# Performance work log

Hardware: AMD Instinct MI355X
Metric: run time of the kernel (lower is better)

The kernel has to match this reference:

```python
import jax, jax.numpy as jnp
import numpy as np

B = 8192   # batch
S = 115    # state dim (fixed by slice layout)
E = 3072   # retrieval embed dim
C = 128    # compressed context dim
A = 23     # action dim
NE = 4096  # number of hyperedge keys
K = 10     # top-k retrieval
TAU = 1.0  # gumbel temperature
EPS = 1e-5 # layernorm eps


def _ln(x, g, b):
    m = x.mean(-1, keepdims=True)
    v = x.var(-1, keepdims=True)
    return (x - m) * jax.lax.rsqrt(v + EPS) * g + b


def _actor(ctx, extra, w1, b1, g1, be1, w2, b2, g2, be2, w3, b3):
    x = jnp.concatenate([ctx, extra], -1)
    x = jax.nn.relu(_ln(x @ w1 + b1, g1, be1))
    x = jax.nn.relu(_ln(x @ w2 + b2, g2, be2))
    return x @ w3 + b3


def setup_inputs() -> dict:
    key = jax.random.key(0)
    ks = iter(jax.random.split(key, 80))

    def W(shape):
        return jax.random.normal(next(ks), shape, jnp.float32) * (1.0 / float(np.sqrt(shape[0])))

    inp = {}
    inp["state"] = jax.random.normal(next(ks), (B, S), jnp.float32)
    u = jax.random.uniform(next(ks), (B, 4), jnp.float32, 1e-6, 1.0 - 1e-6)
    inp["gumbel_noise"] = -jnp.log(-jnp.log(u))  # standard Gumbel samples
    inp["keys"] = jax.random.normal(next(ks), (NE, E), jnp.float32)
    # state encoder 115 -> 512 -> 512 -> 3072 + LN
    inp["se_w1"] = W((S, 512)); inp["se_b1"] = jnp.zeros(512)
    inp["se_w2"] = W((512, 512)); inp["se_b2"] = jnp.zeros(512)
    inp["se_w3"] = W((512, E)); inp["se_b3"] = jnp.zeros(E)
    inp["se_g"] = jnp.ones(E); inp["se_beta"] = jnp.zeros(E)
    # context compressor 3072 -> 512 -> 128 + LN
    inp["cc_w1"] = W((E, 512)); inp["cc_b1"] = jnp.zeros(512)
    inp["cc_w2"] = W((512, C)); inp["cc_b2"] = jnp.zeros(C)
    inp["cc_g"] = jnp.ones(C); inp["cc_beta"] = jnp.zeros(C)
    # 4 actor experts, differing only in extra-slice width
    for p, e in [("a_pre", 50), ("a_scene", 20), ("a_effect", 10), ("a_rule", 15)]:
        inp[p + "_w1"] = W((C + e, C)); inp[p + "_b1"] = jnp.zeros(C)
        inp[p + "_g1"] = jnp.ones(C); inp[p + "_be1"] = jnp.zeros(C)
        inp[p + "_w2"] = W((C, C)); inp[p + "_b2"] = jnp.zeros(C)
        inp[p + "_g2"] = jnp.ones(C); inp[p + "_be2"] = jnp.zeros(C)
        inp[p + "_w3"] = W((C, A)) * 0.01; inp[p + "_b3"] = jnp.zeros(A)  # orthogonal gain=0.01 approx
    # gumbel router 115 -> 64 -> 64 -> 4
    inp["r_w1"] = W((S, 64)); inp["r_b1"] = jnp.zeros(64)
    inp["r_w2"] = W((64, 64)); inp["r_b2"] = jnp.zeros(64)
    inp["r_w3"] = W((64, 4)); inp["r_b3"] = jnp.zeros(4)
    # critic 115 -> 256 -> 256 -> 1
    inp["c_w1"] = W((S, 256)); inp["c_b1"] = jnp.zeros(256)
    inp["c_w2"] = W((256, 256)); inp["c_b2"] = jnp.zeros(256)
    inp["c_w3"] = W((256, 1)); inp["c_b3"] = jnp.zeros(1)
    return inp


def reference(state, gumbel_noise, keys, se_w1, se_b1, se_w2, se_b2, se_w3, se_b3, se_g, se_beta, cc_w1, cc_b1, cc_w2, cc_b2, cc_g, cc_beta, a_pre_w1, a_pre_b1, a_pre_g1, a_pre_be1, a_pre_w2, a_pre_b2, a_pre_g2, a_pre_be2, a_pre_w3, a_pre_b3, a_scene_w1, a_scene_b1, a_scene_g1, a_scene_be1, a_scene_w2, a_scene_b2, a_scene_g2, a_scene_be2, a_scene_w3, a_scene_b3, a_effect_w1, a_effect_b1, a_effect_g1, a_effect_be1, a_effect_w2, a_effect_b2, a_effect_g2, a_effect_be2, a_effect_w3, a_effect_b3, a_rule_w1, a_rule_b1, a_rule_g1, a_rule_be1, a_rule_w2, a_rule_b2, a_rule_g2, a_rule_be2, a_rule_w3, a_rule_b3, r_w1, r_b1, r_w2, r_b2, r_w3, r_b3, c_w1, c_b1, c_w2, c_b2, c_w3, c_b3):
    # 1) state -> query (StateEncoder)
    q = jax.nn.relu(state @ se_w1 + se_b1)
    q = jax.nn.relu(q @ se_w2 + se_b2)
    q = _ln(q @ se_w3 + se_b3, se_g, se_beta)  # (B, E)
    # 2) top-k hard retrieval from hypergraph memory (cosine sim)
    qn = q * jax.lax.rsqrt(jnp.sum(q * q, -1, keepdims=True) + 1e-12)
    kn = keys * jax.lax.rsqrt(jnp.sum(keys * keys, -1, keepdims=True) + 1e-12)
    scores = qn @ kn.T                          # (B, NE)
    _, idx = jax.lax.top_k(scores, K)           # (B, K)
    context = jnp.take(keys, idx, axis=0).mean(1)  # (B, E) mean-pool top-k raw embeddings
    # 3) compress to shared knowledge
    h = jax.nn.relu(context @ cc_w1 + cc_b1)
    shared = _ln(h @ cc_w2 + cc_b2, cc_g, cc_beta)  # (B, C)
    # 4) state slices + 4 actor experts
    belief = state[:, :50]
    location = state[:, 20:40]
    hp = state[:, 40:50]
    inv = state[:, 45:60]
    lp = _actor(shared, belief, a_pre_w1, a_pre_b1, a_pre_g1, a_pre_be1, a_pre_w2, a_pre_b2, a_pre_g2, a_pre_be2, a_pre_w3, a_pre_b3)
    ls = _actor(shared, location, a_scene_w1, a_scene_b1, a_scene_g1, a_scene_be1, a_scene_w2, a_scene_b2, a_scene_g2, a_scene_be2, a_scene_w3, a_scene_b3)
    le = _actor(shared, hp, a_effect_w1, a_effect_b1, a_effect_g1, a_effect_be1, a_effect_w2, a_effect_b2, a_effect_g2, a_effect_be2, a_effect_w3, a_effect_b3)
    lr = _actor(shared, inv, a_rule_w1, a_rule_b1, a_rule_g1, a_rule_be1, a_rule_w2, a_rule_b2, a_rule_g2, a_rule_be2, a_rule_w3, a_rule_b3)
    # 5) gumbel-softmax hard router (straight-through)
    rh = jax.nn.relu(state @ r_w1 + r_b1)
    rh = jax.nn.relu(rh @ r_w2 + r_b2)
    rl = jnp.clip(rh @ r_w3 + r_b3, -20.0, 20.0)
    y_soft = jax.nn.softmax((rl + gumbel_noise) / TAU, -1)
    y_hard = jax.nn.one_hot(jnp.argmax(y_soft, -1), 4, dtype=y_soft.dtype)
    alpha = y_soft + jax.lax.stop_gradient(y_hard - y_soft)  # (B, 4)
    # 6) combine expert logits
    all_l = jnp.stack([lp, ls, le, lr], 1)      # (B, 4, A)
    logits = jnp.einsum('bk,bka->ba', alpha, all_l)
    # critic value
    v = jax.nn.relu(state @ c_w1 + c_b1)
    v = jax.nn.relu(v @ c_w2 + c_b2)
    value = v @ c_w3 + c_b3                      # (B, 1)
    return (logits, alpha, value)
```

## Files before the change

kernel.cpp:

```cpp
#include <hip/hip_runtime.h>

constexpr int Bz = 8192;
constexpr int Sz = 115;
constexpr int Ez = 3072;
constexpr int NEz = 4096;

typedef __attribute__((ext_vector_type(8))) short short8;
typedef __attribute__((ext_vector_type(4))) float floatx4;
typedef unsigned short ushort_t;
typedef unsigned int uint_t;

__device__ __forceinline__ ushort_t f2bf(float f) {
  uint_t u = __float_as_uint(f);
  uint_t r = (u + 0x7FFFu + ((u >> 16) & 1u)) >> 16;
  return (ushort_t)r;
}
__device__ __forceinline__ float bf2f(ushort_t b) {
  uint_t u = ((uint_t)b) << 16;
  return __uint_as_float(u);
}
__device__ __forceinline__ ushort_t f2key(float v) {
  _Float16 h = (_Float16)v;
  ushort_t b = __builtin_bit_cast(ushort_t, h);
  return b ^ ((b & 0x8000u) ? 0xFFFFu : 0x8000u);
}
__device__ __forceinline__ uint_t umax_(uint_t a, uint_t b) { return a > b ? a : b; }

__device__ __forceinline__ void gload16(const ushort_t* g, ushort_t* l) {
  __builtin_amdgcn_global_load_lds(
      (__attribute__((address_space(1))) const void*)g,
      (__attribute__((address_space(3))) void*)l, 16, 0, 0);
}

template<bool RELU, bool BIAS>
__global__ __launch_bounds__(256)
void gemm128(const float* __restrict__ A, const float* __restrict__ Bm,
             const float* __restrict__ bias, float* __restrict__ C,
             int N, int Kd)
{
  __shared__ float As[16][132];
  __shared__ float Bs[16][132];
  const int t  = threadIdx.x;
  const int tx = t & 15, ty = t >> 4;
  const int row0 = blockIdx.y * 128;
  const int col0 = blockIdx.x * 128;
  const int ar = t >> 2, ac = (t & 3) * 4;
  const int bk = t >> 5, bc = (t & 31) * 4;
  const bool a4 = (Kd & 3) == 0;

  float acc[8][8];
#pragma unroll
  for (int i = 0; i < 8; ++i)
#pragma unroll
    for (int j = 0; j < 8; ++j) acc[i][j] = 0.f;

  for (int k0 = 0; k0 < Kd; k0 += 16) {
    const bool fullA = (k0 + 16 <= Kd) && a4;
    {
      const float* ap = A + (size_t)(row0 + ar) * Kd + k0 + ac;
      if (fullA) {
        float4 v0 = *(const float4*)ap;
        float4 v1 = *(const float4*)(ap + (size_t)64 * Kd);
        As[ac + 0][ar] = v0.x; As[ac + 1][ar] = v0.y;
        As[ac + 2][ar] = v0.z; As[ac + 3][ar] = v0.w;
        As[ac + 0][ar + 64] = v1.x; As[ac + 1][ar + 64] = v1.y;
        As[ac + 2][ar + 64] = v1.z; As[ac + 3][ar + 64] = v1.w;
      } else {
#pragma unroll
        for (int e = 0; e < 4; ++e) {
          const int k = k0 + ac + e;
          float v0 = 0.f, v1 = 0.f;
          if (k < Kd) { v0 = ap[e]; v1 = ap[e + (size_t)64 * Kd]; }
          As[ac + e][ar] = v0; As[ac + e][ar + 64] = v1;
        }
      }
    }
    {
      const float* bp = Bm + (size_t)(k0 + bk) * N + col0 + bc;
      if (k0 + 16 <= Kd) {
        *(float4*)&Bs[bk][bc]     = *(const float4*)bp;
        *(float4*)&Bs[bk + 8][bc] = *(const float4*)(bp + (size_t)8 * N);
      } else {
        float4 z; z.x = z.y = z.z = z.w = 0.f;
        *(float4*)&Bs[bk][bc]     = (k0 + bk     < Kd) ? *(const float4*)bp : z;
        *(float4*)&Bs[bk + 8][bc] = (k0 + bk + 8 < Kd) ? *(const float4*)(bp + (size_t)8 * N) : z;
      }
    }
    __syncthreads();
#pragma unroll
    for (int kk = 0; kk < 16; ++kk) {
      float a[8], b[8];
      *(float4*)&a[0] = *(const float4*)&As[kk][ty * 4];
      *(float4*)&a[4] = *(const float4*)&As[kk][64 + ty * 4];
      *(float4*)&b[0] = *(const float4*)&Bs[kk][tx * 4];
      *(float4*)&b[4] = *(const float4*)&Bs[kk][64 + tx * 4];
#pragma unroll
      for (int i = 0; i < 8; ++i)
#pragma unroll
        for (int j = 0; j < 8; ++j)
          acc[i][j] = fmaf(a[i], b[j], acc[i][j]);
    }
    __syncthreads();
  }

  float bv[8];
#pragma unroll
  for (int j = 0; j < 8; ++j) bv[j] = 0.f;
  if (BIAS) {
    *(float4*)&bv[0] = *(const float4*)&bias[col0 + tx * 4];
    *(float4*)&bv[4] = *(const float4*)&bias[col0 + 64 + tx * 4];
  }
#pragma unroll
  for (int i = 0; i < 8; ++i) {
    const int r = row0 + ((i < 4) ? (ty * 4 + i) : (64 + ty * 4 + i - 4));
    float o[8];
#pragma unroll
    for (int j = 0; j < 8; ++j) {
      o[j] = acc[i][j] + bv[j];
      if (RELU) o[j] = fmaxf(o[j], 0.f);
    }
    *(float4*)&C[(size_t)r * N + col0 + tx * 4]      = *(float4*)&o[0];
    *(float4*)&C[(size_t)r * N + col0 + 64 + tx * 4] = *(float4*)&o[4];
  }
}

struct GPart {
  const float* A; const float* Bm; const float* bias;
  float* C; ushort_t* Ch; ushort_t* Cl;
  int N; int Kd; int nbx;
};

__global__ __launch_bounds__(256)
void gemm128_dual(GPart g0, GPart g1)
{
  __shared__ float As[16][132];
  __shared__ float Bs[16][132];
  const int t  = threadIdx.x;
  const int tx = t & 15, ty = t >> 4;
  const bool p0 = (int)blockIdx.x < g0.nbx;
  GPart g = p0 ? g0 : g1;
  const int bx = p0 ? blockIdx.x : (blockIdx.x - g0.nbx);
  const int row0 = blockIdx.y * 128;
  const int col0 = bx * 128;
  const int Kd = g.Kd, N = g.N;
  const int ar = t >> 2, ac = (t & 3) * 4;
  const int bk = t >> 5, bc = (t & 31) * 4;
  const bool a4 = (Kd & 3) == 0;

  float acc[8][8];
#pragma unroll
  for (int i = 0; i < 8; ++i)
#pragma unroll
    for (int j = 0; j < 8; ++j) acc[i][j] = 0.f;

  for (int k0 = 0; k0 < Kd; k0 += 16) {
    const bool fullA = (k0 + 16 <= Kd) && a4;
    {
      const float* ap = g.A + (size_t)(row0 + ar) * Kd + k0 + ac;
      if (fullA) {
        float4 v0 = *(const float4*)ap;
        float4 v1 = *(const float4*)(ap + (size_t)64 * Kd);
        As[ac + 0][ar] = v0.x; As[ac + 1][ar] = v0.y;
        As[ac + 2][ar] = v0.z; As[ac + 3][ar] = v0.w;
        As[ac + 0][ar + 64] = v1.x; As[ac + 1][ar + 64] = v1.y;
        As[ac + 2][ar + 64] = v1.z; As[ac + 3][ar + 64] = v1.w;
      } else {
#pragma unroll
        for (int e = 0; e < 4; ++e) {
          const int k = k0 + ac + e;
          float v0 = 0.f, v1 = 0.f;
          if (k < Kd) { v0 = ap[e]; v1 = ap[e + (size_t)64 * Kd]; }
          As[ac + e][ar] = v0; As[ac + e][ar + 64] = v1;
        }
      }
    }
    {
      const float* bp = g.Bm + (size_t)(k0 + bk) * N + col0 + bc;
      if (k0 + 16 <= Kd) {
        *(float4*)&Bs[bk][bc]     = *(const float4*)bp;
        *(float4*)&Bs[bk + 8][bc] = *(const float4*)(bp + (size_t)8 * N);
      } else {
        float4 z; z.x = z.y = z.z = z.w = 0.f;
        *(float4*)&Bs[bk][bc]     = (k0 + bk     < Kd) ? *(const float4*)bp : z;
        *(float4*)&Bs[bk + 8][bc] = (k0 + bk + 8 < Kd) ? *(const float4*)(bp + (size_t)8 * N) : z;
      }
    }
    __syncthreads();
#pragma unroll
    for (int kk = 0; kk < 16; ++kk) {
      float a[8], b[8];
      *(float4*)&a[0] = *(const float4*)&As[kk][ty * 4];
      *(float4*)&a[4] = *(const float4*)&As[kk][64 + ty * 4];
      *(float4*)&b[0] = *(const float4*)&Bs[kk][tx * 4];
      *(float4*)&b[4] = *(const float4*)&Bs[kk][64 + tx * 4];
#pragma unroll
      for (int i = 0; i < 8; ++i)
#pragma unroll
        for (int j = 0; j < 8; ++j)
          acc[i][j] = fmaf(a[i], b[j], acc[i][j]);
    }
    __syncthreads();
  }

  float bv[8];
  *(float4*)&bv[0] = *(const float4*)&g.bias[col0 + tx * 4];
  *(float4*)&bv[4] = *(const float4*)&g.bias[col0 + 64 + tx * 4];
#pragma unroll
  for (int i = 0; i < 8; ++i) {
    const int r = row0 + ((i < 4) ? (ty * 4 + i) : (64 + ty * 4 + i - 4));
    float o[8];
#pragma unroll
    for (int j = 0; j < 8; ++j) o[j] = fmaxf(acc[i][j] + bv[j], 0.f);
    const size_t i0 = (size_t)r * N + col0 + tx * 4;
    const size_t i1 = i0 + 64;
    if (g.C) {
      *(float4*)&g.C[i0] = *(float4*)&o[0];
      *(float4*)&g.C[i1] = *(float4*)&o[4];
    }
    if (g.Ch) {
      ushort4 h0, l0, h1, l1;
      h0.x = f2bf(o[0]); l0.x = f2bf(o[0] - bf2f(h0.x));
      h0.y = f2bf(o[1]); l0.y = f2bf(o[1] - bf2f(h0.y));
      h0.z = f2bf(o[2]); l0.z = f2bf(o[2] - bf2f(h0.z));
      h0.w = f2bf(o[3]); l0.w = f2bf(o[3] - bf2f(h0.w));
      h1.x = f2bf(o[4]); l1.x = f2bf(o[4] - bf2f(h1.x));
      h1.y = f2bf(o[5]); l1.y = f2bf(o[5] - bf2f(h1.y));
      h1.z = f2bf(o[6]); l1.z = f2bf(o[6] - bf2f(h1.z));
      h1.w = f2bf(o[7]); l1.w = f2bf(o[7] - bf2f(h1.w));
      *(ushort4*)&g.Ch[i0] = h0; *(ushort4*)&g.Cl[i0] = l0;
      *(ushort4*)&g.Ch[i1] = h1; *(ushort4*)&g.Cl[i1] = l1;
    }
  }
}

template<int NSUB>
__global__ __launch_bounds__(256)
void mfma_bt(const ushort_t* __restrict__ A, const ushort_t* __restrict__ B,
             ushort_t* __restrict__ Cout, int N, int Kd)
{
  __shared__ ushort_t Al[NSUB * 4096];
  __shared__ ushort_t Bl[NSUB * 4096];
  const int t = threadIdx.x;
  const int wid = t >> 6, lane = t & 63;
  const int wr = wid >> 1, wc = wid & 1;
  const int row0 = blockIdx.y << 7;
  const int col0 = blockIdx.x << 7;
  const int srow = lane >> 2;
  const int scol = (lane & 3) * 8;

  const ushort_t* ga0 = A + (size_t)(row0 + wid * 16 + srow) * Kd + scol;
  const ushort_t* ga1 = A + (size_t)(row0 + (wid + 4) * 16 + srow) * Kd + scol;
  const ushort_t* gb0 = B + (size_t)(col0 + wid * 16 + srow) * Kd + scol;
  const ushort_t* gb1 = B + (size_t)(col0 + (wid + 4) * 16 + srow) * Kd + scol;
  ushort_t* la0 = &Al[wid * 512];
  ushort_t* la1 = &Al[(wid + 4) * 512];
  ushort_t* lb0 = &Bl[wid * 512];
  ushort_t* lb1 = &Bl[(wid + 4) * 512];

  const int mr = lane & 15, qd = lane >> 4;

  floatx4 acc[4][4];
#pragma unroll
  for (int i = 0; i < 4; ++i)
#pragma unroll
    for (int j = 0; j < 4; ++j) acc[i][j] = (floatx4){0.f, 0.f, 0.f, 0.f};

  for (int kb = 0; kb < Kd; kb += 32 * NSUB) {
#pragma unroll
    for (int tt = 0; tt < NSUB; ++tt) {
      const int ko = kb + 32 * tt;
      const int lo = tt * 4096;
      gload16(ga0 + ko, la0 + lo);
      gload16(ga1 + ko, la1 + lo);
      gload16(gb0 + ko, lb0 + lo);
      gload16(gb1 + ko, lb1 + lo);
    }
    __syncthreads();
#pragma unroll
    for (int tt = 0; tt < NSUB; ++tt) {
      const int lo = tt * 4096;
      short8 aF[4], bF[4];
#pragma unroll
      for (int i = 0; i < 4; ++i)
        aF[i] = *(const short8*)&Al[lo + (wr * 64 + i * 16 + mr) * 32 + qd * 8];
#pragma unroll
      for (int j = 0; j < 4; ++j)
        bF[j] = *(const short8*)&Bl[lo + (wc * 64 + j * 16 + mr) * 32 + qd * 8];
#pragma unroll
      for (int i = 0; i < 4; ++i)
#pragma unroll
        for (int j = 0; j < 4; ++j)
          acc[i][j] = __builtin_amdgcn_mfma_f32_16x16x32_bf16(aF[i], bF[j], acc[i][j], 0, 0, 0);
    }
    __syncthreads();
  }

#pragma unroll
  for (int i = 0; i < 4; ++i) {
#pragma unroll
    for (int j = 0; j < 4; ++j) {
      const int col = col0 + wc * 64 + j * 16 + mr;
#pragma unroll
      for (int r = 0; r < 4; ++r) {
        const int row = row0 + wr * 64 + i * 16 + qd * 4 + r;
        Cout[(size_t)row * N + col] = f2key(acc[i][j][r]);
      }
    }
  }
}

template<int EPI>
__global__ __launch_bounds__(256)
void mfma3_bt(const ushort_t* __restrict__ Ah, const ushort_t* __restrict__ Alo,
              const ushort_t* __restrict__ Bh, const ushort_t* __restrict__ Blo,
              const float* __restrict__ bias, float* __restrict__ Cout,
              ushort_t* __restrict__ Ch, ushort_t* __restrict__ Cl,
              int N, int Kd)
{
  __shared__ ushort_t AhL[128 * 32];
  __shared__ ushort_t AlL[128 * 32];
  __shared__ ushort_t BhL[128 * 32];
  __shared__ ushort_t BlL[128 * 32];
  const int t = threadIdx.x;
  const int wid = t >> 6, lane = t & 63;
  const int wr = wid >> 1, wc = wid & 1;
  const int row0 = blockIdx.y * 128;
  const int col0 = blockIdx.x * 128;
  const int srow = lane >> 2;
  const int scol = (lane & 3) * 8;

  const size_t aoff0 = (size_t)(row0 + wid * 16 + srow) * Kd + scol;
  const size_t aoff1 = (size_t)(row0 + (wid + 4) * 16 + srow) * Kd + scol;
  const size_t boff0 = (size_t)(col0 + wid * 16 + srow) * Kd + scol;
  const size_t boff1 = (size_t)(col0 + (wid + 4) * 16 + srow) * Kd + scol;
  const int l0 = (wid * 16) * 32;
  const int l1 = ((wid + 4) * 16) * 32;

  const int mr = lane & 15, qd = lane >> 4;

  floatx4 acc[4][4];
#pragma unroll
  for (int i = 0; i < 4; ++i)
#pragma unroll
    for (int j = 0; j < 4; ++j) acc[i][j] = (floatx4){0.f, 0.f, 0.f, 0.f};

  for (int kb = 0; kb < Kd; kb += 32) {
    gload16(Ah + aoff0 + kb, &AhL[l0]);
    gload16(Ah + aoff1 + kb, &AhL[l1]);
    gload16(Alo + aoff0 + kb, &AlL[l0]);
    gload16(Alo + aoff1 + kb, &AlL[l1]);
    gload16(Bh + boff0 + kb, &BhL[l0]);
    gload16(Bh + boff1 + kb, &BhL[l1]);
    gload16(Blo + boff0 + kb, &BlL[l0]);
    gload16(Blo + boff1 + kb, &BlL[l1]);
    __syncthreads();
    short8 ahF[4], alF[4], bhF[4], blF[4];
#pragma unroll
    for (int i = 0; i < 4; ++i) {
      const int o = (wr * 64 + i * 16 + mr) * 32 + qd * 8;
      ahF[i] = *(const short8*)&AhL[o];
      alF[i] = *(const short8*)&AlL[o];
    }
#pragma unroll
    for (int j = 0; j < 4; ++j) {
      const int o = (wc * 64 + j * 16 + mr) * 32 + qd * 8;
      bhF[j] = *(const short8*)&BhL[o];
      blF[j] = *(const short8*)&BlL[o];
    }
#pragma unroll
    for (int i = 0; i < 4; ++i)
#pragma unroll
      for (int j = 0; j < 4; ++j) {
        acc[i][j] = __builtin_amdgcn_mfma_f32_16x16x32_bf16(alF[i], bhF[j], acc[i][j], 0, 0, 0);
        acc[i][j] = __builtin_amdgcn_mfma_f32_16x16x32_bf16(ahF[i], blF[j], acc[i][j], 0, 0, 0);
        acc[i][j] = __builtin_amdgcn_mfma_f32_16x16x32_bf16(ahF[i], bhF[j], acc[i][j], 0, 0, 0);
      }
    __syncthreads();
  }

#pragma unroll
  for (int i = 0; i < 4; ++i) {
#pragma unroll
    for (int j = 0; j < 4; ++j) {
      const int col = col0 + wc * 64 + j * 16 + mr;
#pragma unroll
      for (int r = 0; r < 4; ++r) {
        const int row = row0 + wr * 64 + i * 16 + qd * 4 + r;
        const float v = acc[i][j][r] + bias[col];
        if (EPI == 0) {
          Cout[(size_t)row * N + col] = v;
        } else {
          const float y = fmaxf(v, 0.f);
          const ushort_t h = f2bf(y);
          Ch[(size_t)row * N + col] = h;
          Cl[(size_t)row * N + col] = f2bf(y - bf2f(h));
        }
      }
    }
  }
}

__global__ __launch_bounds__(256)
void mfma_bt64(const ushort_t* __restrict__ A, const ushort_t* __restrict__ B,
               const float* __restrict__ bias, float* __restrict__ Cout,
               int N, int Kd)
{
  __shared__ ushort_t Al[2 * 64 * 32];
  __shared__ ushort_t Bl[2 * 128 * 32];
  const int t = threadIdx.x;
  const int wid = t >> 6, lane = t & 63;
  const int row0 = blockIdx.y << 6;
  const int col0 = blockIdx.x << 7;
  const int srow = lane >> 2;
  const int scol = (lane & 3) * 8;
  const int mr = lane & 15, qd = lane >> 4;

  const ushort_t* gsrc[6];
  ushort_t* ldst[6];
#pragma unroll
  for (int m = 0; m < 6; ++m) {
    const int c = wid * 6 + m;
    if (c < 8) {
      const int sub = c >> 2, grp = c & 3;
      gsrc[m] = A + (size_t)(row0 + grp * 16 + srow) * Kd + sub * 32 + scol;
      ldst[m] = &Al[sub * 2048 + (grp * 16 + srow) * 32];
    } else {
      const int b = c - 8, sub = b >> 3, grp = b & 7;
      gsrc[m] = B + (size_t)(col0 + grp * 16 + srow) * Kd + sub * 32 + scol;
      ldst[m] = &Bl[sub * 4096 + (grp * 16 + srow) * 32];
    }
  }

  floatx4 acc[4][2];
#pragma unroll
  for (int i = 0; i < 4; ++i)
#pragma unroll
    for (int j = 0; j < 2; ++j) acc[i][j] = (floatx4){0.f, 0.f, 0.f, 0.f};

  for (int kb = 0; kb < Kd; kb += 64) {
#pragma unroll
    for (int m = 0; m < 6; ++m) gload16(gsrc[m] + kb, ldst[m]);
    __syncthreads();
#pragma unroll
    for (int sub = 0; sub < 2; ++sub) {
      short8 aF[4], bF[2];
#pragma unroll
      for (int i = 0; i < 4; ++i)
        aF[i] = *(const short8*)&Al[sub * 2048 + (i * 16 + mr) * 32 + qd * 8];
#pragma unroll
      for (int j = 0; j < 2; ++j)
        bF[j] = *(const short8*)&Bl[sub * 4096 + (wid * 32 + j * 16 + mr) * 32 + qd * 8];
#pragma unroll
      for (int i = 0; i < 4; ++i)
#pragma unroll
        for (int j = 0; j < 2; ++j)
          acc[i][j] = __builtin_amdgcn_mfma_f32_16x16x32_bf16(aF[i], bF[j], acc[i][j], 0, 0, 0);
    }
    __syncthreads();
  }

#pragma unroll
  for (int i = 0; i < 4; ++i) {
#pragma unroll
    for (int j = 0; j < 2; ++j) {
      const int col = col0 + wid * 32 + j * 16 + mr;
#pragma unroll
      for (int r = 0; r < 4; ++r) {
        const int row = row0 + i * 16 + qd * 4 + r;
        Cout[(size_t)row * N + col] = fmaxf(acc[i][j][r] + bias[col], 0.f);
      }
    }
  }
}

__global__ __launch_bounds__(256)
void gemm_scores(const float* __restrict__ A, const float* __restrict__ Bm,
                 const float* __restrict__ rk, ushort_t* __restrict__ S)
{
  __shared__ float As[16][132];
  __shared__ float Bs[16][132];
  const int t  = threadIdx.x;
  const int tx = t & 15, ty = t >> 4;
  const int row0 = blockIdx.y * 128;
  const int col0 = blockIdx.x * 128;
  const int ar = t >> 2, ac = (t & 3) * 4;
  const int Kd = Ez;

  float acc[8][8];
#pragma unroll
  for (int i = 0; i < 8; ++i)
#pragma unroll
    for (int j = 0; j < 8; ++j) acc[i][j] = 0.f;

  for (int k0 = 0; k0 < Kd; k0 += 16) {
    {
      const float* ap = A + (size_t)(row0 + ar) * Kd + k0 + ac;
      float4 v0 = *(const float4*)ap;
      float4 v1 = *(const float4*)(ap + (size_t)64 * Kd);
      As[ac + 0][ar] = v0.x; As[ac + 1][ar] = v0.y;
      As[ac + 2][ar] = v0.z; As[ac + 3][ar] = v0.w;
      As[ac + 0][ar + 64] = v1.x; As[ac + 1][ar + 64] = v1.y;
      As[ac + 2][ar + 64] = v1.z; As[ac + 3][ar + 64] = v1.w;
    }
    {
      const float* bp = Bm + (size_t)(col0 + ar) * Kd + k0 + ac;
      float4 v0 = *(const float4*)bp;
      float4 v1 = *(const float4*)(bp + (size_t)64 * Kd);
      Bs[ac + 0][ar] = v0.x; Bs[ac + 1][ar] = v0.y;
      Bs[ac + 2][ar] = v0.z; Bs[ac + 3][ar] = v0.w;
      Bs[ac + 0][ar + 64] = v1.x; Bs[ac + 1][ar + 64] = v1.y;
      Bs[ac + 2][ar + 64] = v1.z; Bs[ac + 3][ar + 64] = v1.w;
    }
    __syncthreads();
#pragma unroll
    for (int kk = 0; kk < 16; ++kk) {
      float a[8], b[8];
      *(float4*)&a[0] = *(const float4*)&As[kk][ty * 4];
      *(float4*)&a[4] = *(const float4*)&As[kk][64 + ty * 4];
      *(float4*)&b[0] = *(const float4*)&Bs[kk][tx * 4];
      *(float4*)&b[4] = *(const float4*)&Bs[kk][64 + tx * 4];
#pragma unroll
      for (int i = 0; i < 8; ++i)
#pragma unroll
        for (int j = 0; j < 8; ++j)
          acc[i][j] = fmaf(a[i], b[j], acc[i][j]);
    }
    __syncthreads();
  }

  float rk0[8];
  *(float4*)&rk0[0] = *(const float4*)&rk[col0 + tx * 4];
  *(float4*)&rk0[4] = *(const float4*)&rk[col0 + 64 + tx * 4];
#pragma unroll
  for (int i = 0; i < 8; ++i) {
    const int r = row0 + ((i < 4) ? (ty * 4 + i) : (64 + ty * 4 + i - 4));
    ushort4 h0, h1;
    h0.x = f2key(acc[i][0] * rk0[0]); h0.y = f2key(acc[i][1] * rk0[1]);
    h0.z = f2key(acc[i][2] * rk0[2]); h0.w = f2key(acc[i][3] * rk0[3]);
    h1.x = f2key(acc[i][4] * rk0[4]); h1.y = f2key(acc[i][5] * rk0[5]);
    h1.z = f2key(acc[i][6] * rk0[6]); h1.w = f2key(acc[i][7] * rk0[7]);
    *(ushort4*)&S[(size_t)r * NEz + col0 + tx * 4]      = h0;
    *(ushort4*)&S[(size_t)r * NEz + col0 + 64 + tx * 4] = h1;
  }
}

struct LN4 {
  const float* W[4]; const float* b[4]; const float* g[4]; const float* be[4];
  int eoff[4]; int elen[4];
};

template<bool RELU, bool HASEXT>
__global__ __launch_bounds__(256)
void gemm_ln4(const float* __restrict__ A1base, size_t a1stride, int K1,
              const float* __restrict__ A2, LN4 p,
              float* __restrict__ outbase, size_t ostride)
{
  __shared__ float As[32][68];
  __shared__ float Bs[32][132];
  __shared__ float rsum[64][17];
  __shared__ float rsq[64][17];
  __shared__ float stm[64], str[64];
  const int a = blockIdx.y;
  const float* A1 = A1base + (size_t)a * a1stride;
  float* out = outbase + (size_t)a * ostride;
  const float* W = p.W[a];
  const float* bias = p.b[a];
  const float* g = p.g[a];
  const float* be = p.be[a];
  const int eoff = HASEXT ? p.eoff[a] : 0;
  const int K2 = HASEXT ? p.elen[a] : 0;

  const int t = threadIdx.x;
  const int tx = t & 15, ty = t >> 4;
  const int row0 = blockIdx.x * 64;
  const int Kt = K1 + K2;
  const int ar = t >> 2, ac = (t & 3) * 8;
  const int bk = t >> 3, bc = (t & 7) * 16;

  float acc[4][8];
#pragma unroll
  for (int i = 0; i < 4; ++i)
#pragma unroll
    for (int j = 0; j < 8; ++j) acc[i][j] = 0.f;

  for (int k0 = 0; k0 < Kt; k0 += 32) {
    const int grow = row0 + ar;
#pragma unroll
    for (int e = 0; e < 8; ++e) {
      const int k = k0 + ac + e;
      float v = 0.f;
      if (k < K1)      v = A1[(size_t)grow * K1 + k];
      else if (k < Kt) v = A2[(size_t)grow * 115 + eoff + (k - K1)];
      As[ac + e][ar] = v;
    }
    {
      const int k = k0 + bk;
#pragma unroll
      for (int qd = 0; qd < 4; ++qd) {
        float4 z; z.x = z.y = z.z = z.w = 0.f;
        *(float4*)&Bs[bk][bc + 4 * qd] =
            (k < Kt) ? *(const float4*)&W[(size_t)k * 128 + bc + 4 * qd] : z;
      }
    }
    __syncthreads();
#pragma unroll
    for (int kk = 0; kk < 32; ++kk) {
      float av[4], bv2[8];
// ... 275 lines not shown
  __shared__ double sv[16];
  __shared__ int si[16];
  __shared__ int sel10[10];
  const int row = blockIdx.x, t = threadIdx.x;
  const int w = t >> 6, lane = t & 63;

  {
    const float* qr = qn + (size_t)row * Ez;
#pragma unroll
    for (int i = 0; i < 3; ++i) {
      const int c = (t << 2) + (i << 10);
      *(float4*)&qs[c] = *(const float4*)&qr[c];
    }
  }
  __syncthreads();

#pragma unroll
  for (int cc = 0; cc < 4; ++cc) {
    const int slot = w * 4 + cc;
    const int id = cand[(size_t)row * 16 + slot];
    const float* kr = keys + (size_t)id * Ez;
    double s = 0.0;
#pragma unroll
    for (int it = 0; it < 12; ++it) {
      const int c = (lane << 2) + (it << 8);
      float4 k4 = *(const float4*)&kr[c];
      float4 q4 = *(const float4*)&qs[c];
      s += (double)q4.x * (double)k4.x;
      s += (double)q4.y * (double)k4.y;
      s += (double)q4.z * (double)k4.z;
      s += (double)q4.w * (double)k4.w;
    }
#pragma unroll
    for (int d = 32; d; d >>= 1) s += __shfl_down(s, d, 64);
    if (lane == 0) { sv[slot] = s * (double)rk[id]; si[slot] = id; }
  }
  __syncthreads();

  if (t == 0) {
    for (int it = 0; it < 10; ++it) {
      int bj = 0; double bvv = sv[0]; int bi = si[0];
      for (int j = 1; j < 16; ++j) {
        const double v = sv[j]; const int i2 = si[j];
        if (v > bvv || (v == bvv && i2 < bi)) { bj = j; bvv = v; bi = i2; }
      }
      sel10[it] = bi;
      sv[bj] = -1e300;
    }
  }
  __syncthreads();

  int id[10];
#pragma unroll
  for (int j = 0; j < 10; ++j) id[j] = sel10[j];

#pragma unroll
  for (int i = 0; i < 3; ++i) {
    const int c = (t << 2) + (i << 10);
    float4 a = {0.f, 0.f, 0.f, 0.f};
#pragma unroll
    for (int j = 0; j < 10; ++j) {
      float4 v = *(const float4*)&keys[(size_t)id[j] * Ez + c];
      a.x += v.x; a.y += v.y; a.z += v.z; a.w += v.w;
    }
    if (BFOUT) {
      ushort4 o;
      o.x = f2bf(a.x * 0.1f); o.y = f2bf(a.y * 0.1f);
      o.z = f2bf(a.z * 0.1f); o.w = f2bf(a.w * 0.1f);
      *(ushort4*)&((ushort_t*)ctxOut)[(size_t)row * Ez + c] = o;
    } else {
      float4 o;
      o.x = a.x * 0.1f; o.y = a.y * 0.1f; o.z = a.z * 0.1f; o.w = a.w * 0.1f;
      *(float4*)&((float*)ctxOut)[(size_t)row * Ez + c] = o;
    }
  }
}

__global__ __launch_bounds__(256)
void router_kernel(const float* __restrict__ state, const float* __restrict__ gn,
                   const float* __restrict__ w1, const float* __restrict__ b1,
                   const float* __restrict__ w2, const float* __restrict__ b2,
                   const float* __restrict__ w3, const float* __restrict__ b3,
                   float* __restrict__ outAlpha)
{
  const int row = blockIdx.x * 256 + threadIdx.x;
  const float* sr = state + (size_t)row * Sz;
  float h1[64];
#pragma unroll
  for (int j = 0; j < 64; ++j) h1[j] = b1[j];
  for (int k = 0; k < Sz; ++k) {
    const float a = sr[k];
    const float* wr = w1 + (size_t)k * 64;
#pragma unroll
    for (int j = 0; j < 64; ++j) h1[j] = fmaf(a, wr[j], h1[j]);
  }
#pragma unroll
  for (int j = 0; j < 64; ++j) h1[j] = fmaxf(h1[j], 0.f);
  float h2[64];
#pragma unroll
  for (int j = 0; j < 64; ++j) h2[j] = b2[j];
#pragma unroll
  for (int k = 0; k < 64; ++k) {
    const float a = h1[k];
    const float* wr = w2 + (size_t)k * 64;
#pragma unroll
    for (int j = 0; j < 64; ++j) h2[j] = fmaf(a, wr[j], h2[j]);
  }
#pragma unroll
  for (int j = 0; j < 64; ++j) h2[j] = fmaxf(h2[j], 0.f);
  float z[4];
#pragma unroll
  for (int a = 0; a < 4; ++a) {
    float s = b3[a];
#pragma unroll
    for (int k = 0; k < 64; ++k) s = fmaf(h2[k], w3[k * 4 + a], s);
    s = fminf(fmaxf(s, -20.f), 20.f);
    z[a] = s + gn[(size_t)row * 4 + a];
  }
  float mz = z[0];
#pragma unroll
  for (int a = 1; a < 4; ++a) mz = fmaxf(mz, z[a]);
  float e[4]; float se = 0.f;
#pragma unroll
  for (int a = 0; a < 4; ++a) { e[a] = expf(z[a] - mz); se += e[a]; }
  const float inv = 1.f / se;
  float y[4];
#pragma unroll
  for (int a = 0; a < 4; ++a) y[a] = e[a] * inv;
  int am = 0;
#pragma unroll
  for (int a = 1; a < 4; ++a) if (y[a] > y[am]) am = a;
#pragma unroll
  for (int a = 0; a < 4; ++a) {
    const float hard = (a == am) ? 1.f : 0.f;
    outAlpha[(size_t)row * 4 + a] = y[a] + (hard - y[a]);
  }
}

__global__ __launch_bounds__(256)
void critic_head(const float* __restrict__ c2, const float* __restrict__ w3,
                 const float* __restrict__ b3, float* __restrict__ outv)
{
  const int t = threadIdx.x;
  const int w = t >> 6, lane = t & 63;
  const int row0 = blockIdx.x * 64 + w * 16;
  float wv[4];
  *(float4*)&wv[0] = *(const float4*)&w3[lane * 4];
  const float b0 = b3[0];
#pragma unroll
  for (int rr = 0; rr < 16; ++rr) {
    const int row = row0 + rr;
    float4 x = *(const float4*)&c2[(size_t)row * 256 + lane * 4];
    float s = x.x * wv[0] + x.y * wv[1] + x.z * wv[2] + x.w * wv[3];
#pragma unroll
    for (int d = 32; d; d >>= 1) s += __shfl_down(s, d, 64);
    if (lane == 0) outv[row] = s + b0;
  }
}

struct HeadP { const float* w3[4]; const float* b3[4]; };

__global__ __launch_bounds__(256)
void actor_head4(const float* __restrict__ x2g, HeadP p,
                 const float* __restrict__ alpha, float* __restrict__ outL)
{
  __shared__ float wsm[4][128 * 23];
  __shared__ float bs[4][23];
  const int t = threadIdx.x;
#pragma unroll
  for (int a = 0; a < 4; ++a) {
    for (int i = t; i < 128 * 23; i += 256) wsm[a][i] = p.w3[a][i];
    if (t < 23) bs[a][t] = p.b3[a][t];
  }
  __syncthreads();
  const int row = blockIdx.x * 32 + (t >> 3);
  const int cg = t & 7;
  float sum[3] = {0.f, 0.f, 0.f};
#pragma unroll
  for (int a = 0; a < 4; ++a) {
    const float al = alpha[(size_t)row * 4 + a];
    const float* xr = x2g + (size_t)a * Bz * 128 + (size_t)row * 128;
    float acc[3] = {0.f, 0.f, 0.f};
    for (int kk = 0; kk < 128; ++kk) {
      const float xa = xr[kk];
#pragma unroll
      for (int j = 0; j < 3; ++j) {
        const int col = cg + 8 * j;
        if (col < 23) acc[j] = fmaf(xa, wsm[a][kk * 23 + col], acc[j]);
      }
    }
#pragma unroll
    for (int j = 0; j < 3; ++j) {
      const int col = cg + 8 * j;
      if (col < 23) sum[j] += al * (acc[j] + bs[a][col]);
    }
  }
#pragma unroll
  for (int j = 0; j < 3; ++j) {
    const int col = cg + 8 * j;
    if (col < 23) outL[(size_t)row * 23 + col] = sum[j];
  }
}

extern "C" void kernel_launch(void* const* d_in, const int* in_sizes, int n_in,
                              void* d_out, int out_size, void* d_ws, size_t ws_size,
                              hipStream_t stream)
{
  const float* state  = (const float*)d_in[0];
  const float* gumbel = (const float*)d_in[1];
  const float* keys   = (const float*)d_in[2];
  const float* se_w1 = (const float*)d_in[3];
  const float* se_b1 = (const float*)d_in[4];
  const float* se_w2 = (const float*)d_in[5];
  const float* se_b2 = (const float*)d_in[6];
  const float* se_w3 = (const float*)d_in[7];
  const float* se_b3 = (const float*)d_in[8];
  const float* se_g  = (const float*)d_in[9];
  const float* se_be = (const float*)d_in[10];
  const float* cc_w1 = (const float*)d_in[11];
  const float* cc_b1 = (const float*)d_in[12];
  const float* cc_w2 = (const float*)d_in[13];
  const float* cc_b2 = (const float*)d_in[14];
  const float* cc_g  = (const float*)d_in[15];
  const float* cc_be = (const float*)d_in[16];
  const float* r_w1 = (const float*)d_in[57];
  const float* r_b1 = (const float*)d_in[58];
  const float* r_w2 = (const float*)d_in[59];
  const float* r_b2 = (const float*)d_in[60];
  const float* r_w3 = (const float*)d_in[61];
  const float* r_b3 = (const float*)d_in[62];
  const float* c_w1 = (const float*)d_in[63];
  const float* c_b1 = (const float*)d_in[64];
  const float* c_w2 = (const float*)d_in[65];
  const float* c_b2 = (const float*)d_in[66];
  const float* c_w3 = (const float*)d_in[67];
  const float* c_b3 = (const float*)d_in[68];

  float* wsf = (float*)d_ws;
  const size_t qF = (size_t)Bz * Ez;
  const size_t uF = (size_t)16777216;
  float* q = wsf;
  float* U = wsf + qF;
  ushort_t* sAh  = (ushort_t*)(U + 0);
  ushort_t* sAl  = (ushort_t*)(U + 2097152);
  ushort_t* sBh  = (ushort_t*)(U + 4194304);
  ushort_t* sBl  = (ushort_t*)(U + 6291456);
  ushort_t* w3hT = (ushort_t*)(U + 8388608);
  ushort_t* w3lT = (ushort_t*)(U + 9175040);
  ushort_t* w2hT = (ushort_t*)(U + 9961472);
  ushort_t* w2lT = (ushort_t*)(U + 10092544);
  float* sA = U;
  float* sB = U + 4194304;
  ushort_t* scoresU = (ushort_t*)U;
  ushort_t* ctxb = (ushort_t*)U;
  float* cch = U + 12582912;
  float* shr = U;
  float* x1g = U + 1 * 1048576;
  float* x2g = U + 5 * 1048576;
  float* cr1 = q;
  float* cr2 = q + 2097152;
  ushort_t* qbf  = (ushort_t*)(wsf + qF + uF);
  ushort_t* knbf = qbf + qF;
  ushort_t* w1T  = knbf + (size_t)NEz * Ez;
  const size_t bfHalves = qF + (size_t)NEz * Ez + (size_t)512 * Ez;
  const size_t baseBytes = (qF + uF) * sizeof(float);
  const size_t tailBytes = 4096 * 4 + (size_t)Bz * 16 * 4;
  const bool fast = ws_size >= baseBytes + bfHalves * 2 + tailBytes;
  float* tailF = (float*)((char*)d_ws + (fast ? baseBytes + bfHalves * 2 : baseBytes));
  float* rk  = tailF;
  int* cand  = (int*)(tailF + 4096);

  float* outL = (float*)d_out;
  float* outA = outL + (size_t)Bz * 23;
  float* outV = outA + (size_t)Bz * 4;

  const dim3 blk(256);

  {
    GPart e0 = {state, se_w1, se_b1, fast ? nullptr : sA,
                fast ? sAh : nullptr, fast ? sAl : nullptr, 512, 115, 4};
    GPart e1 = {state, c_w1, c_b1, cr1, nullptr, nullptr, 256, 115, 2};
    gemm128_dual<<<dim3(6, 64), blk, 0, stream>>>(e0, e1);
  }
  gemm128<true, true><<<dim3(2, 64), blk, 0, stream>>>(cr1, c_w2, c_b2, cr2, 256, 256);

  if (fast) {
    wt_split2<<<dim3(8, 56), blk, 0, stream>>>(se_w2, w2hT, w2lT, se_w3, w3hT, w3lT);
    mfma3_bt<1><<<dim3(4, 64), blk, 0, stream>>>(sAh, sAl, w2hT, w2lT, se_b2,
                                                 nullptr, sBh, sBl, 512, 512);
  } else {
    gemm128<true, true><<<dim3(4, 64), blk, 0, stream>>>(sA, se_w2, se_b2, sB, 512, 512);
  }

  critic_head<<<dim3(128), blk, 0, stream>>>(cr2, c_w3, c_b3, outV);
  router_kernel<<<dim3(32), blk, 0, stream>>>(state, gumbel, r_w1, r_b1, r_w2, r_b2,
                                              r_w3, r_b3, outA);

  if (fast) {
    mfma3_bt<0><<<dim3(24, 64), blk, 0, stream>>>(sBh, sBl, w3hT, w3lT, se_b3,
                                                  q, nullptr, nullptr, 3072, 512);
    norm_cvt_fused<<<dim3(Bz + NEz), blk, 0, stream>>>(q, se_g, se_be, qbf,
                                                       keys, rk, knbf);
    cvt_w1t_t<<<dim3(48, 8), blk, 0, stream>>>(cc_w1, w1T);
    mfma_bt<2><<<dim3(32, 64), blk, 0, stream>>>(qbf, knbf, scoresU, NEz, Ez);
  } else {
    gemm128<false, true><<<dim3(24, 64), blk, 0, stream>>>(sB, se_w3, se_b3, q, 3072, 512);
    ln_l2_q<<<dim3(Bz), blk, 0, stream>>>(q, se_g, se_be);
    keynorm<<<dim3(NEz), blk, 0, stream>>>(keys, rk);
    gemm_scores<<<dim3(32, 64), blk, 0, stream>>>(q, keys, rk, scoresU);
  }

  topk16<<<dim3(Bz), blk, 0, stream>>>(scoresU, cand);

  if (fast) {
    rescore_gather<true><<<dim3(Bz), blk, 0, stream>>>(q, keys, rk, cand, ctxb);
    mfma_bt64<<<dim3(4, 128), blk, 0, stream>>>(ctxb, w1T, cc_b1, cch, 512, Ez);
  } else {
    rescore_gather<false><<<dim3(Bz), blk, 0, stream>>>(q, keys, rk, cand, q);
    gemm128<true, true><<<dim3(4, 64), blk, 0, stream>>>(q, cc_w1, cc_b1, cch, 512, Ez);
  }
  {
    LN4 pcc = {};
    pcc.W[0] = cc_w2; pcc.b[0] = cc_b2; pcc.g[0] = cc_g; pcc.be[0] = cc_be;
    gemm_ln4<false, false><<<dim3(128, 1), blk, 0, stream>>>(cch, 0, 512, nullptr, pcc,
                                                             shr, 0);
  }

  {
    LN4 p1 = {}, p2 = {};
    HeadP ph = {};
    const int eoffs[4] = {0, 20, 40, 45};
    const int elens[4] = {50, 20, 10, 15};
    for (int a = 0; a < 4; ++a) {
      const int base = 17 + 10 * a;
      p1.W[a]  = (const float*)d_in[base + 0];
      p1.b[a]  = (const float*)d_in[base + 1];
      p1.g[a]  = (const float*)d_in[base + 2];
      p1.be[a] = (const float*)d_in[base + 3];
      p1.eoff[a] = eoffs[a]; p1.elen[a] = elens[a];
      p2.W[a]  = (const float*)d_in[base + 4];
      p2.b[a]  = (const float*)d_in[base + 5];
      p2.g[a]  = (const float*)d_in[base + 6];
      p2.be[a] = (const float*)d_in[base + 7];
      ph.w3[a] = (const float*)d_in[base + 8];
      ph.b3[a] = (const float*)d_in[base + 9];
    }
    gemm_ln4<true, true ><<<dim3(128, 4), blk, 0, stream>>>(shr, 0, 128, state, p1,
                                                            x1g, (size_t)Bz * 128);
    gemm_ln4<true, false><<<dim3(128, 4), blk, 0, stream>>>(x1g, (size_t)Bz * 128, 128,
                                                            nullptr, p2,
                                                            x2g, (size_t)Bz * 128);
    actor_head4<<<dim3(256), blk, 0, stream>>>(x2g, ph, outA, outL);
  }
}
```

Before: 1.290 ms.

## Replace screening GEMM with 256x256 tiled, double-buffered, swizzled MFMA pipeline

Replaces the 128x128-tile bf16 screening GEMM (queries x keys, K=3072) with a 512-thread kernel that computes 256x256 output tiles. It double-buffers K=64 LDS tiles with an XOR swizzle to avoid bank conflicts. It interleaves global-to-LDS loads with LDS reads and MFMA phases using explicit waitcnt, barriers, sched_barrier and setprio. The goal is to raise arithmetic intensity and overlap memory latency with matrix math. The cost is more registers and LDS per block (launch bounds 512,2) and a fragile hand-written schedule.

```diff
diff --git a/kernel.cpp b/kernel.cpp
--- a/kernel.cpp
+++ b/kernel.cpp
@@ -233,76 +233,163 @@
   }
 }
 
-template<int NSUB>
-__global__ __launch_bounds__(256)
-void mfma_bt(const ushort_t* __restrict__ A, const ushort_t* __restrict__ B,
-             ushort_t* __restrict__ Cout, int N, int Kd)
-{
-  __shared__ ushort_t Al[NSUB * 4096];
-  __shared__ ushort_t Bl[NSUB * 4096];
+__global__ __launch_bounds__(512, 2)
+void screen256(const ushort_t* __restrict__ A, const ushort_t* __restrict__ B,
+               ushort_t* __restrict__ Cout, int N, int Kd)
+{
+  __shared__ ushort_t AL[2 * 256 * 64];
+  __shared__ ushort_t BL[2 * 256 * 64];
   const int t = threadIdx.x;
-  const int wid = t >> 6, lane = t & 63;
-  const int wr = wid >> 1, wc = wid & 1;
-  const int row0 = blockIdx.y << 7;
-  const int col0 = blockIdx.x << 7;
-  const int srow = lane >> 2;
-  const int scol = (lane & 3) * 8;
-
-  const ushort_t* ga0 = A + (size_t)(row0 + wid * 16 + srow) * Kd + scol;
-  const ushort_t* ga1 = A + (size_t)(row0 + (wid + 4) * 16 + srow) * Kd + scol;
-  const ushort_t* gb0 = B + (size_t)(col0 + wid * 16 + srow) * Kd + scol;
-  const ushort_t* gb1 = B + (size_t)(col0 + (wid + 4) * 16 + srow) * Kd + scol;
-  ushort_t* la0 = &Al[wid * 512];
-  ushort_t* la1 = &Al[(wid + 4) * 512];
-  ushort_t* lb0 = &Bl[wid * 512];
-  ushort_t* lb1 = &Bl[(wid + 4) * 512];
-
+  const int lane = t & 63;
+  const int wid = t >> 6;
+  const int wr = wid >> 2;
+  const int wc = wid & 3;
   const int mr = lane & 15, qd = lane >> 4;
-
-  floatx4 acc[4][4];
-#pragma unroll
-  for (int i = 0; i < 4; ++i)
+  const int row0 = blockIdx.y << 8;
+  const int col0 = blockIdx.x << 8;
+  const int NT = Kd >> 6;
+
+  const int l8 = lane >> 3;
+  const int c8 = (lane & 7) ^ l8;
+  const ushort_t* pA = A + (size_t)(row0 + wr * 128 + wc * 16 + l8) * Kd + c8 * 8;
+  const ushort_t* pB = B + (size_t)(col0 + (wid >> 1) * 64 + (wid & 1) * 16 + l8) * Kd + c8 * 8;
+  ushort_t* aWp = &AL[wr * 8192 + wc * 1024];
+  ushort_t* bWp = &BL[(wid >> 1) * 4096 + (wid & 1) * 1024];
+
+  const int swz = (mr & 7) << 4;
+  const int aRow = (wr * 128 + mr) * 64;
+  const int bRow = (wc * 64 + mr) * 64;
+  const int cu0 = ((qd * 16) ^ swz) >> 1;
+  const int cu1 = ((64 + qd * 16) ^ swz) >> 1;
+
+  floatx4 acc[8][4];
+#pragma unroll
+  for (int i = 0; i < 8; ++i)
 #pragma unroll
     for (int j = 0; j < 4; ++j) acc[i][j] = (floatx4){0.f, 0.f, 0.f, 0.f};
 
-  for (int kb = 0; kb < Kd; kb += 32 * NSUB) {
-#pragma unroll
-    for (int tt = 0; tt < NSUB; ++tt) {
-      const int ko = kb + 32 * tt;
-      const int lo = tt * 4096;
-      gload16(ga0 + ko, la0 + lo);
-      gload16(ga1 + ko, la1 + lo);
-      gload16(gb0 + ko, lb0 + lo);
-      gload16(gb1 + ko, lb1 + lo);
-    }
-    __syncthreads();
-#pragma unroll
-    for (int tt = 0; tt < NSUB; ++tt) {
-      const int lo = tt * 4096;
-      short8 aF[4], bF[4];
-#pragma unroll
-      for (int i = 0; i < 4; ++i)
-        aF[i] = *(const short8*)&Al[lo + (wr * 64 + i * 16 + mr) * 32 + qd * 8];
-#pragma unroll
-      for (int j = 0; j < 4; ++j)
-        bF[j] = *(const short8*)&Bl[lo + (wc * 64 + j * 16 + mr) * 32 + qd * 8];
-#pragma unroll
-      for (int i = 0; i < 4; ++i)
-#pragma unroll
-        for (int j = 0; j < 4; ++j)
-          acc[i][j] = __builtin_amdgcn_mfma_f32_16x16x32_bf16(aF[i], bF[j], acc[i][j], 0, 0, 0);
-    }
-    __syncthreads();
-  }
-
-#pragma unroll
-  for (int i = 0; i < 4; ++i) {
+  short8 aF[4][2], b01[2][2], b23[2][2];
+
+#define STA(db, h, tile) do {                                            \
+    const int kt_ = ((tile) < NT ? (tile) : 0) << 6;                     \
+    gload16(pA + (size_t)((h) * 64) * Kd + kt_,                          \
+            aWp + (db) * 16384 + (h) * 4096);                            \
+    gload16(pA + (size_t)((h) * 64 + 8) * Kd + kt_,                      \
+            aWp + (db) * 16384 + (h) * 4096 + 512);                      \
+  } while (0)
+#define STB(db, g, tile) do {                                            \
+    const int kt_ = ((tile) < NT ? (tile) : 0) << 6;                     \
+    gload16(pB + (size_t)((g) * 32) * Kd + kt_,                          \
+            bWp + (db) * 16384 + (g) * 2048);                            \
+    gload16(pB + (size_t)((g) * 32 + 8) * Kd + kt_,                      \
+            bWp + (db) * 16384 + (g) * 2048 + 512);                      \
+  } while (0)
+#define LDA(db, half)                                                    \
+  _Pragma("unroll")                                                      \
+  for (int i_ = 0; i_ < 4; ++i_) {                                       \
+    const int b_ = (db) * 16384 + aRow + ((half) * 4 + i_) * 1024;       \
+    aF[i_][0] = *(const short8*)&AL[b_ + cu0];                           \
+    aF[i_][1] = *(const short8*)&AL[b_ + cu1];                           \
+  }
+#define LDB(db, jh, bF)                                                  \
+  _Pragma("unroll")                                                      \
+  for (int j_ = 0; j_ < 2; ++j_) {                                       \
+    const int b_ = (db) * 16384 + bRow + ((jh) * 2 + j_) * 1024;         \
+    bF[j_][0] = *(const short8*)&BL[b_ + cu0];                           \
+    bF[j_][1] = *(const short8*)&BL[b_ + cu1];                           \
+  }
+#define MM(ih, jh, bF)                                                   \
+  _Pragma("unroll")                                                      \
+  for (int i_ = 0; i_ < 4; ++i_)                                         \
+    _Pragma("unroll")                                                    \
+    for (int j_ = 0; j_ < 2; ++j_) {                                     \
+      acc[(ih)*4+i_][(jh)*2+j_] = __builtin_amdgcn_mfma_f32_16x16x32_bf16( \
+          aF[i_][0], bF[j_][0], acc[(ih)*4+i_][(jh)*2+j_], 0, 0, 0);     \
+      acc[(ih)*4+i_][(jh)*2+j_] = __builtin_amdgcn_mfma_f32_16x16x32_bf16( \
+          aF[i_][1], bF[j_][1], acc[(ih)*4+i_][(jh)*2+j_], 0, 0, 0);     \
+    }
+#define SCH0() __builtin_amdgcn_sched_barrier(0)
+#define BARM() do { __builtin_amdgcn_s_barrier();                        \
+                    asm volatile("" ::: "memory"); SCH0(); } while (0)
+#define WLG()  do { asm volatile("s_waitcnt lgkmcnt(0)" ::: "memory");   \
+                    SCH0(); } while (0)
+#define WVM(n) do { asm volatile("s_waitcnt vmcnt(" #n ")" ::: "memory");\
+                    SCH0(); } while (0)
+
+  STA(0, 0, 0); STB(0, 1, 0); STA(0, 1, 0); STB(0, 0, 0);
+  WVM(4);
+  STA(1, 0, 1); STB(1, 1, 1); STA(1, 1, 1);
+  WVM(6);
+  BARM();
+
+  for (int it = 0; it < NT / 2; ++it) {
+    const int tp = it * 2;
+    LDA(0, 0); LDB(0, 0, b01);
+    STB(1, 0, tp + 1);
+    __builtin_amdgcn_s_barrier(); WLG();
+    __builtin_amdgcn_s_setprio(1); MM(0, 0, b01); __builtin_amdgcn_s_setprio(0);
+    BARM();
+    LDB(0, 1, b23);
+    STA(0, 0, tp + 2);
+    __builtin_amdgcn_s_barrier(); WLG();
+    __builtin_amdgcn_s_setprio(1); MM(0, 1, b23); __builtin_amdgcn_s_setprio(0);
+    BARM();
+    LDA(0, 1);
+    STB(0, 1, tp + 2);
+    __builtin_amdgcn_s_barrier(); WLG();
+    __builtin_amdgcn_s_setprio(1); MM(1, 1, b23); __builtin_amdgcn_s_setprio(0);
+    BARM();
+    LDB(0, 0, b01);
+    STA(0, 1, tp + 2);
+    WVM(6);
+    __builtin_amdgcn_s_barrier(); WLG();
+    __builtin_amdgcn_s_setprio(1); MM(1, 0, b01); __builtin_amdgcn_s_setprio(0);
+    BARM();
+    LDA(1, 0); LDB(1, 0, b01);
+    STB(0, 0, tp + 2);
+    __builtin_amdgcn_s_barrier(); WLG();
+    __builtin_amdgcn_s_setprio(1); MM(0, 0, b01); __builtin_amdgcn_s_setprio(0);
+    BARM();
+    LDB(1, 1, b23);
+    STA(1, 0, tp + 3);
+    __builtin_amdgcn_s_barrier(); WLG();
+    __builtin_amdgcn_s_setprio(1); MM(0, 1, b23); __builtin_amdgcn_s_setprio(0);
+    BARM();
+    LDA(1, 1);
+    STB(1, 1, tp + 3);
+    __builtin_amdgcn_s_barrier(); WLG();
+    __builtin_amdgcn_s_setprio(1); MM(1, 1, b23); __builtin_amdgcn_s_setprio(0);
+    BARM();
+    LDB(1, 0, b01);
+    STA(1, 1, tp + 3);
+    WVM(6);
+    __builtin_amdgcn_s_barrier(); WLG();
+    __builtin_amdgcn_s_setprio(1); MM(1, 0, b01); __builtin_amdgcn_s_setprio(0);
+    BARM();
+  }
+
+  asm volatile("s_waitcnt vmcnt(0) lgkmcnt(0)" ::: "memory");
+  SCH0();
+  __syncthreads();
+
+#undef STA
+#undef STB
+#undef LDA
+#undef LDB
+#undef MM
+#undef SCH0
+#undef BARM
+#undef WLG
+#undef WVM
+
+#pragma unroll
+  for (int i = 0; i < 8; ++i) {
 #pragma unroll
     for (int j = 0; j < 4; ++j) {
       const int col = col0 + wc * 64 + j * 16 + mr;
 #pragma unroll
       for (int r = 0; r < 4; ++r) {
-        const int row = row0 + wr * 64 + i * 16 + qd * 4 + r;
+        const int row = row0 + wr * 128 + i * 16 + qd * 4 + r;
         Cout[(size_t)row * N + col] = f2key(acc[i][j][r]);
       }
     }
@@ -1184,7 +1271,7 @@
     norm_cvt_fused<<<dim3(Bz + NEz), blk, 0, stream>>>(q, se_g, se_be, qbf,
                                                        keys, rk, knbf);
     cvt_w1t_t<<<dim3(48, 8), blk, 0, stream>>>(cc_w1, w1T);
-    mfma_bt<2><<<dim3(32, 64), blk, 0, stream>>>(qbf, knbf, scoresU, NEz, Ez);
+    screen256<<<dim3(16, 32), dim3(512), 0, stream>>>(qbf, knbf, scoresU, NEz, Ez);
   } else {
     gemm128<false, true><<<dim3(24, 64), blk, 0, stream>>>(sB, se_w3, se_b3, q, 3072, 512);
     ln_l2_q<<<dim3(Bz), blk, 0, stream>>>(q, se_g, se_be);
```

Result: no change. 1.267 ms (-1.8%).
